# Optimization experiments

Hardware: AMD Instinct MI355X
Metric: run time of the kernel (lower is better)

## Reference

```python
import jax, jax.numpy as jnp
import numpy as np

T, B, I, H = 2048, 512, 10, 20  # seq_len, batch, input_size, hidden_size
G = 4 * H  # gate dim, PyTorch order: i, f, g, o


def _lstm_scan(x, w_ih, w_hh, b_ih, b_hh):
    # x: [T, B, I]; w_ih: [4H, I]; w_hh: [4H, H]; biases: [4H]
    # Precompute input projection for all timesteps (one big GEMM).
    x_proj = jnp.einsum('tbi,gi->tbg', x, w_ih) + b_ih + b_hh  # [T, B, 4H]

    def step(carry, xg):
        h, c = carry
        gates = xg + h @ w_hh.T  # [B, 4H]
        i, f, g, o = jnp.split(gates, 4, axis=-1)
        i = jax.nn.sigmoid(i)
        f = jax.nn.sigmoid(f)
        g = jnp.tanh(g)
        o = jax.nn.sigmoid(o)
        c = f * c + i * g
        h = o * jnp.tanh(c)
        return (h, c), h

    h0 = jnp.zeros((x.shape[1], H), x.dtype)
    c0 = jnp.zeros((x.shape[1], H), x.dtype)
    _, hs = jax.lax.scan(step, (h0, c0), x_proj)
    return hs  # [T, B, H]


def setup_inputs() -> dict:
    key = jax.random.key(0)
    ks = jax.random.split(key, 9)
    s_ih = 1.0 / np.sqrt(H)
    inp = {
        'x': jax.random.normal(ks[0], (T, B, I, 1), dtype=jnp.float32),
        'w_ih_f': jax.random.uniform(ks[1], (G, I), jnp.float32, -s_ih, s_ih),
        'w_hh_f': jax.random.uniform(ks[2], (G, H), jnp.float32, -s_ih, s_ih),
        'b_ih_f': jax.random.uniform(ks[3], (G,), jnp.float32, -s_ih, s_ih),
        'b_hh_f': jax.random.uniform(ks[4], (G,), jnp.float32, -s_ih, s_ih),
        'w_ih_r': jax.random.uniform(ks[5], (G, I), jnp.float32, -s_ih, s_ih),
        'w_hh_r': jax.random.uniform(ks[6], (G, H), jnp.float32, -s_ih, s_ih),
        'b_ih_r': jax.random.uniform(ks[7], (G,), jnp.float32, -s_ih, s_ih),
        'b_hh_r': jax.random.uniform(ks[8], (G,), jnp.float32, -s_ih, s_ih),
    }
    return inp


def reference(x, w_ih_f, w_hh_f, b_ih_f, b_hh_f, w_ih_r, w_hh_r, b_ih_r, b_hh_r):
    xs = jnp.squeeze(x, -1)  # [T, B, I]
    out_f = _lstm_scan(xs, w_ih_f, w_hh_f, b_ih_f, b_hh_f)            # forward dir
    out_r = _lstm_scan(xs[::-1], w_ih_r, w_hh_r, b_ih_r, b_hh_r)[::-1]  # reverse dir
    return jnp.concatenate([out_f, out_r], axis=-1)  # [T, B, 2H]
```

## Files before the change

kernel.cpp:

```cpp
#include <hip/hip_runtime.h>

typedef float f2 __attribute__((ext_vector_type(2)));
typedef float f4 __attribute__((ext_vector_type(4)));

#define TT 2048
#define BB 512
#define II 10
#define HH 20
#define CH 16
#define RS 32
#define NCHUNK (TT / CH)

#define LOG2E 1.44269504088896340736f

__device__ __forceinline__ float fexp2(float x) {
#if __has_builtin(__builtin_amdgcn_exp2f)
    return __builtin_amdgcn_exp2f(x);
#else
    return exp2f(x);
#endif
}

__global__ __launch_bounds__(128) void lstm_bidir(
    const float* __restrict__ x,
    const float* __restrict__ w_ih_f, const float* __restrict__ w_hh_f,
    const float* __restrict__ b_ih_f, const float* __restrict__ b_hh_f,
    const float* __restrict__ w_ih_r, const float* __restrict__ w_hh_r,
    const float* __restrict__ b_ih_r, const float* __restrict__ b_hh_r,
    float* __restrict__ out)
{
    const int tid  = threadIdx.x;
    const int wid  = tid >> 6;
    const int lane = tid & 63;
    const int s    = blockIdx.x;

    const int  dirh = lane >> 5;
    const int  hl   = lane & 31;
    const bool valid = (hl < HH);
    const int  j     = valid ? hl : (HH - 1);

    const float* __restrict__ w_ih = dirh ? w_ih_r : w_ih_f;
    const float* __restrict__ w_hh = dirh ? w_hh_r : w_hh_f;
    const float* __restrict__ b_ih = dirh ? b_ih_r : b_ih_f;
    const float* __restrict__ b_hh = dirh ? b_hh_r : b_hh_f;

    const int t0    = dirh ? (TT - 1) : 0;
    const int xstep = dirh ? -(BB * II) : (BB * II);
    const int ostep = dirh ? -(BB * 2 * HH) : (BB * 2 * HH);
    const int xbase = (t0 * BB + s) * II;

    const float gsc[4] = { -LOG2E, -LOG2E, -2.0f * LOG2E, -LOG2E };

    __shared__ f4    ring[RS][64];
    __shared__ float hstage[CH * 64];

    if (wid == 1) {
        f2 wih[4][5];
        float bs[4];
#pragma unroll
        for (int g = 0; g < 4; ++g) {
            const int r = g * HH + j;
#pragma unroll
            for (int k = 0; k < 5; ++k) {
                f2 w = *(const f2*)(w_ih + r * II + 2 * k);
                wih[g][k] = w * gsc[g];
            }
            bs[g] = (b_ih[r] + b_hh[r]) * gsc[g];
        }

        auto produce8 = [&](int base) {
            f2 xb[8][5];
#pragma unroll
            for (int i = 0; i < 8; ++i) {
                int u = base + i; if (u > TT - 1) u = TT - 1;
                const float* px = x + (xbase + u * xstep);
#pragma unroll
                for (int k = 0; k < 5; ++k) xb[i][k] = *(const f2*)(px + 2 * k);
            }
#pragma unroll
            for (int i = 0; i < 8; ++i) {
                const int u = base + i;
                if (u < TT) {
                    f4 xp;
#pragma unroll
                    for (int g = 0; g < 4; ++g) {
                        f2 p = {bs[g], 0.f};
#pragma unroll
                        for (int k = 0; k < 5; ++k) p += wih[g][k] * xb[i][k];
                        xp[g] = p[0] + p[1];
                    }
                    ring[u & (RS - 1)][lane] = xp;
                }
            }
        };

        produce8(0);
        produce8(8);
        for (int chunk = 0; chunk < NCHUNK; ++chunk) {
            __syncthreads();
            const int base = (chunk + 1) * CH;
            produce8(base);
            produce8(base + 8);
        }
    } else {
        __builtin_amdgcn_s_setprio(1);

        f2 whh[4][10];
#pragma unroll
        for (int g = 0; g < 4; ++g) {
            const int r = g * HH + j;
#pragma unroll
            for (int k = 0; k < 10; ++k) {
                f2 w = *(const f2*)(w_hh + r * HH + 2 * k);
                whh[g][k] = w * gsc[g];
            }
        }

        const int obase = (t0 * BB + s) * (2 * HH) + dirh * HH;
        int offd[10], lds_d[10];
#pragma unroll
        for (int q = 0; q < 10; ++q) {
            const int idx = q * 32 + hl;
            const int td  = idx / HH;
            const int jd  = idx - td * HH;
            offd[q]  = obase + td * ostep + jd;
            lds_d[q] = td * 64 + dirh * 32 + jd;
        }

        const int hboff = dirh * 32;

        f4 hb[5];
#pragma unroll
        for (int k = 0; k < 5; ++k) hb[k] = f4{0.f, 0.f, 0.f, 0.f};

        float c = 0.0f, h = 0.0f;
        int t = 0;

        for (int chunk = 0; chunk < NCHUNK; ++chunk) {
            __syncthreads();
            f4 xp = ring[t & (RS - 1)][lane];
#pragma unroll
            for (int i = 0; i < CH; ++i, ++t) {
                f2 a0[4], a1[4];
#pragma unroll
                for (int g = 0; g < 4; ++g) { a0[g] = f2{0.f, 0.f}; a1[g] = f2{0.f, 0.f}; }
#pragma unroll
                for (int k = 0; k < 5; ++k) {
                    const f4 hv = hb[k];
                    f2 lo; lo[0] = hv[0]; lo[1] = hv[1];
                    f2 hi; hi[0] = hv[2]; hi[1] = hv[3];
#pragma unroll
                    for (int g = 0; g < 4; ++g) {
                        a0[g] += whh[g][2 * k]     * lo;
                        a1[g] += whh[g][2 * k + 1] * hi;
                    }
                }
                float u[4];
#pragma unroll
                for (int g = 0; g < 4; ++g) {
                    const f2 a = a0[g] + a1[g];
                    u[g] = (xp[g] + a[0]) + a[1];
                }

                const float ig = __builtin_amdgcn_rcpf(1.0f + fexp2(u[0]));
                const float fg = __builtin_amdgcn_rcpf(1.0f + fexp2(u[1]));
                const float sg = __builtin_amdgcn_rcpf(1.0f + fexp2(u[2]));
                const float og = __builtin_amdgcn_rcpf(1.0f + fexp2(u[3]));
                const float i2 = ig + ig;
                const float o2 = og + og;

                const float m = __builtin_fmaf(i2, sg, -ig);
                c = __builtin_fmaf(fg, c, m);
                const float sc_ = __builtin_amdgcn_rcpf(
                                    1.0f + fexp2(c * (-2.0f * LOG2E)));
                h = __builtin_fmaf(o2, sc_, -og);

                hstage[i * 64 + lane] = h;
                __builtin_amdgcn_wave_barrier();

#pragma unroll
                for (int k = 0; k < 5; ++k)
                    hb[k] = *(const f4*)&hstage[i * 64 + hboff + 4 * k];

                if (i < CH - 1) xp = ring[(t + 1) & (RS - 1)][lane];
            }

#pragma unroll
            for (int q = 0; q < 10; ++q) {
                const float v = hstage[lds_d[q]];
                out[offd[q]] = v;
                offd[q] += CH * ostep;
            }
        }
    }
}

extern "C" void kernel_launch(void* const* d_in, const int* in_sizes, int n_in,
                              void* d_out, int out_size, void* d_ws, size_t ws_size,
                              hipStream_t stream) {
    const float* xp     = (const float*)d_in[0];
    const float* w_ih_f = (const float*)d_in[1];
    const float* w_hh_f = (const float*)d_in[2];
    const float* b_ih_f = (const float*)d_in[3];
    const float* b_hh_f = (const float*)d_in[4];
    const float* w_ih_r = (const float*)d_in[5];
    const float* w_hh_r = (const float*)d_in[6];
    const float* b_ih_r = (const float*)d_in[7];
    const float* b_hh_r = (const float*)d_in[8];
    float* outp = (float*)d_out;

    hipLaunchKernelGGL(lstm_bidir, dim3(512), dim3(128), 0, stream,
                       xp, w_ih_f, w_hh_f, b_ih_f, b_hh_f,
                       w_ih_r, w_hh_r, b_ih_r, b_hh_r, outp);
}
```

Baseline: 506.7 us.

## Interleave forward and reverse LSTM recurrences within each lane of the consumer wave

Each consumer lane used to handle a single direction, with lanes 0-31 forward and 32-63 reverse. Now every lane computes both directions, holding both hidden weight sets (whhA/whhB) and staging each direction's h in its own LDS half. The two independent dependency chains are interleaved so one can hide the other's latency. The cost is roughly double the per-lane arithmetic, since all 64 lanes now do redundant work, plus heavier register pressure, and launch_bounds(128,1) is added to permit that.

```diff
diff --git a/kernel.cpp b/kernel.cpp
--- a/kernel.cpp
+++ b/kernel.cpp
@@ -21,7 +21,7 @@
 #endif
 }
 
-__global__ __launch_bounds__(128) void lstm_bidir(
+__global__ __launch_bounds__(128, 1) void lstm_bidir(
     const float* __restrict__ x,
     const float* __restrict__ w_ih_f, const float* __restrict__ w_hh_f,
     const float* __restrict__ b_ih_f, const float* __restrict__ b_hh_f,
@@ -34,27 +34,23 @@
     const int lane = tid & 63;
     const int s    = blockIdx.x;
 
-    const int  dirh = lane >> 5;
-    const int  hl   = lane & 31;
-    const bool valid = (hl < HH);
-    const int  j     = valid ? hl : (HH - 1);
-
-    const float* __restrict__ w_ih = dirh ? w_ih_r : w_ih_f;
-    const float* __restrict__ w_hh = dirh ? w_hh_r : w_hh_f;
-    const float* __restrict__ b_ih = dirh ? b_ih_r : b_ih_f;
-    const float* __restrict__ b_hh = dirh ? b_hh_r : b_hh_f;
-
-    const int t0    = dirh ? (TT - 1) : 0;
-    const int xstep = dirh ? -(BB * II) : (BB * II);
-    const int ostep = dirh ? -(BB * 2 * HH) : (BB * 2 * HH);
-    const int xbase = (t0 * BB + s) * II;
+    const bool valid = ((lane & 31) < HH);
+    const int  j     = valid ? (lane & 31) : (HH - 1);
 
     const float gsc[4] = { -LOG2E, -LOG2E, -2.0f * LOG2E, -LOG2E };
 
     __shared__ f4    ring[RS][64];
-    __shared__ float hstage[CH * 64];
+    __shared__ float hstage[2 * CH * 64];
 
     if (wid == 1) {
+        const int dirh = lane >> 5;
+        const float* __restrict__ w_ih = dirh ? w_ih_r : w_ih_f;
+        const float* __restrict__ b_ih = dirh ? b_ih_r : b_ih_f;
+        const float* __restrict__ b_hh = dirh ? b_hh_r : b_hh_f;
+        const int t0    = dirh ? (TT - 1) : 0;
+        const int xstep = dirh ? -(BB * II) : (BB * II);
+        const int xbase = (t0 * BB + s) * II;
+
         f2 wih[4][5];
         float bs[4];
 #pragma unroll
@@ -105,91 +101,109 @@
     } else {
         __builtin_amdgcn_s_setprio(1);
 
-        f2 whh[4][10];
+        f2 whhA[4][10], whhB[4][10];
 #pragma unroll
         for (int g = 0; g < 4; ++g) {
             const int r = g * HH + j;
 #pragma unroll
             for (int k = 0; k < 10; ++k) {
-                f2 w = *(const f2*)(w_hh + r * HH + 2 * k);
-                whh[g][k] = w * gsc[g];
-            }
-        }
-
-        const int obase = (t0 * BB + s) * (2 * HH) + dirh * HH;
-        int offd[10], lds_d[10];
-#pragma unroll
-        for (int q = 0; q < 10; ++q) {
-            const int idx = q * 32 + hl;
-            const int td  = idx / HH;
-            const int jd  = idx - td * HH;
-            offd[q]  = obase + td * ostep + jd;
-            lds_d[q] = td * 64 + dirh * 32 + jd;
-        }
-
-        const int hboff = dirh * 32;
-
-        f4 hb[5];
-#pragma unroll
-        for (int k = 0; k < 5; ++k) hb[k] = f4{0.f, 0.f, 0.f, 0.f};
-
-        float c = 0.0f, h = 0.0f;
+                f2 wA = *(const f2*)(w_hh_f + r * HH + 2 * k);
+                f2 wB = *(const f2*)(w_hh_r + r * HH + 2 * k);
+                whhA[g][k] = wA * gsc[g];
+                whhB[g][k] = wB * gsc[g];
+            }
+        }
+
+        const int ostepF = BB * 2 * HH;
+        const int ostepR = -ostepF;
+        const int obaseF = s * 2 * HH;
+        const int obaseR = ((TT - 1) * BB + s) * 2 * HH + HH;
+
+        auto comp = [&](const f2 (&whh)[4][10], const f4 (&hb)[5], const f4& xp,
+                        float& c, float& h) {
+            f2 a0[4], a1[4];
+#pragma unroll
+            for (int g = 0; g < 4; ++g) { a0[g] = f2{xp[g], 0.f}; a1[g] = f2{0.f, 0.f}; }
+#pragma unroll
+            for (int k = 0; k < 5; ++k) {
+                const f4 hv = hb[k];
+                f2 lo; lo[0] = hv[0]; lo[1] = hv[1];
+                f2 hi; hi[0] = hv[2]; hi[1] = hv[3];
+#pragma unroll
+                for (int g = 0; g < 4; ++g) {
+                    a0[g] += whh[g][2 * k]     * lo;
+                    a1[g] += whh[g][2 * k + 1] * hi;
+                }
+            }
+            float u[4];
+#pragma unroll
+            for (int g = 0; g < 4; ++g) {
+                const f2 a = a0[g] + a1[g];
+                u[g] = a[0] + a[1];
+            }
+            const float ig = __builtin_amdgcn_rcpf(1.0f + fexp2(u[0]));
+            const float fg = __builtin_amdgcn_rcpf(1.0f + fexp2(u[1]));
+            const float sg = __builtin_amdgcn_rcpf(1.0f + fexp2(u[2]));
+            const float og = __builtin_amdgcn_rcpf(1.0f + fexp2(u[3]));
+            const float i2 = ig + ig;
+            const float o2 = og + og;
+            const float m  = __builtin_fmaf(i2, sg, -ig);
+            c = __builtin_fmaf(fg, c, m);
+            const float sc_ = __builtin_amdgcn_rcpf(
+                                1.0f + fexp2(c * (-2.0f * LOG2E)));
+            h = __builtin_fmaf(o2, sc_, -og);
+        };
+
+        hstage[CH * 64 + (CH - 1) * 64 + lane] = 0.0f;
+
+        f4 hbA[5], hbB[5];
+#pragma unroll
+        for (int k = 0; k < 5; ++k) hbA[k] = f4{0.f, 0.f, 0.f, 0.f};
+
+        float cA = 0.f, hA = 0.f, cB = 0.f, hB = 0.f;
         int t = 0;
 
         for (int chunk = 0; chunk < NCHUNK; ++chunk) {
             __syncthreads();
-            f4 xp = ring[t & (RS - 1)][lane];
+            f4 xpA = ring[t & (RS - 1)][j];
+            f4 xpB = ring[t & (RS - 1)][32 + j];
 #pragma unroll
             for (int i = 0; i < CH; ++i, ++t) {
-                f2 a0[4], a1[4];
-#pragma unroll
-                for (int g = 0; g < 4; ++g) { a0[g] = f2{0.f, 0.f}; a1[g] = f2{0.f, 0.f}; }
-#pragma unroll
-                for (int k = 0; k < 5; ++k) {
-                    const f4 hv = hb[k];
-                    f2 lo; lo[0] = hv[0]; lo[1] = hv[1];
-                    f2 hi; hi[0] = hv[2]; hi[1] = hv[3];
-#pragma unroll
-                    for (int g = 0; g < 4; ++g) {
-                        a0[g] += whh[g][2 * k]     * lo;
-                        a1[g] += whh[g][2 * k + 1] * hi;
-                    }
+#pragma unroll
+                for (int k = 0; k < 5; ++k)
+                    hbB[k] = *(const f4*)&hstage[CH * 64 + (((i + CH - 1) & (CH - 1)) * 64) + 4 * k];
+
+                comp(whhA, hbA, xpA, cA, hA);
+
+                hstage[i * 64 + lane] = hA;
+                __builtin_amdgcn_wave_barrier();
+
+#pragma unroll
+                for (int k = 0; k < 5; ++k)
+                    hbA[k] = *(const f4*)&hstage[i * 64 + 4 * k];
+
+                comp(whhB, hbB, xpB, cB, hB);
+
+                hstage[CH * 64 + i * 64 + lane] = hB;
+                __builtin_amdgcn_wave_barrier();
+
+                if (i < CH - 1) {
+                    xpA = ring[(t + 1) & (RS - 1)][j];
+                    xpB = ring[(t + 1) & (RS - 1)][32 + j];
                 }
-                float u[4];
-#pragma unroll
-                for (int g = 0; g < 4; ++g) {
-                    const f2 a = a0[g] + a1[g];
-                    u[g] = (xp[g] + a[0]) + a[1];
-                }
-
-                const float ig = __builtin_amdgcn_rcpf(1.0f + fexp2(u[0]));
-                const float fg = __builtin_amdgcn_rcpf(1.0f + fexp2(u[1]));
-                const float sg = __builtin_amdgcn_rcpf(1.0f + fexp2(u[2]));
-                const float og = __builtin_amdgcn_rcpf(1.0f + fexp2(u[3]));
-                const float i2 = ig + ig;
-                const float o2 = og + og;
-
-                const float m = __builtin_fmaf(i2, sg, -ig);
-                c = __builtin_fmaf(fg, c, m);
-                const float sc_ = __builtin_amdgcn_rcpf(
-                                    1.0f + fexp2(c * (-2.0f * LOG2E)));
-                h = __builtin_fmaf(o2, sc_, -og);
-
-                hstage[i * 64 + lane] = h;
-                __builtin_amdgcn_wave_barrier();
-
-#pragma unroll
-                for (int k = 0; k < 5; ++k)
-                    hb[k] = *(const f4*)&hstage[i * 64 + hboff + 4 * k];
-
-                if (i < CH - 1) xp = ring[(t + 1) & (RS - 1)][lane];
             }
 
 #pragma unroll
             for (int q = 0; q < 10; ++q) {
-                const float v = hstage[lds_d[q]];
-                out[offd[q]] = v;
-                offd[q] += CH * ostep;
+                const int sc  = q / 5;
+                const int idx = (q % 5) * 64 + lane;
+                const int td  = idx / HH;
+                const int jd  = idx - td * HH;
+                const float v = hstage[sc * CH * 64 + td * 64 + jd];
+                const int tglob = chunk * CH + td;
+                const int o = sc ? (obaseR + tglob * ostepR + jd)
+                                 : (obaseF + tglob * ostepF + jd);
+                out[o] = v;
             }
         }
     }
```

Result: slower. 780.3 us (+54.0%).

## Process two batch sequences per block with interleaved recurrences for ILP

Applied to the files above, without the earlier changes.

Each block now handles two batch elements, so grid size halves to 256 blocks. The compute wave runs two independent LSTM recurrences in alternation, letting one chain's dependent latency (LDS round-trip, transcendentals) overlap with the other's arithmetic. The input projection is also folded into the accumulator init, and the output store is reorganised to write both sequences' rows together. The cost is twice the serial work per wave, so the kernel only gains if the interleaving hides enough of each step's latency, and the halved grid may leave CUs idle.

```diff
diff --git a/kernel.cpp b/kernel.cpp
--- a/kernel.cpp
+++ b/kernel.cpp
@@ -21,7 +21,7 @@
 #endif
 }
 
-__global__ __launch_bounds__(128) void lstm_bidir(
+__global__ __launch_bounds__(128, 1) void lstm_bidir(
     const float* __restrict__ x,
     const float* __restrict__ w_ih_f, const float* __restrict__ w_hh_f,
     const float* __restrict__ b_ih_f, const float* __restrict__ b_hh_f,
@@ -32,12 +32,19 @@
     const int tid  = threadIdx.x;
     const int wid  = tid >> 6;
     const int lane = tid & 63;
-    const int s    = blockIdx.x;
-
-    const int  dirh = lane >> 5;
-    const int  hl   = lane & 31;
+    const int blk  = blockIdx.x;
+    const int sA   = 2 * blk;
+    const int sB   = 2 * blk + 1;
+
+    const int  dirh  = lane >> 5;
+    const int  hl    = lane & 31;
     const bool valid = (hl < HH);
     const int  j     = valid ? hl : (HH - 1);
+
+    const float gsc[4] = { -LOG2E, -LOG2E, -2.0f * LOG2E, -LOG2E };
+
+    __shared__ f4    ring[RS][2][64];
+    __shared__ float hstage[2][CH][64];
 
     const float* __restrict__ w_ih = dirh ? w_ih_r : w_ih_f;
     const float* __restrict__ w_hh = dirh ? w_hh_r : w_hh_f;
@@ -46,13 +53,6 @@
 
     const int t0    = dirh ? (TT - 1) : 0;
     const int xstep = dirh ? -(BB * II) : (BB * II);
-    const int ostep = dirh ? -(BB * 2 * HH) : (BB * 2 * HH);
-    const int xbase = (t0 * BB + s) * II;
-
-    const float gsc[4] = { -LOG2E, -LOG2E, -2.0f * LOG2E, -LOG2E };
-
-    __shared__ f4    ring[RS][64];
-    __shared__ float hstage[CH * 64];
 
     if (wid == 1) {
         f2 wih[4][5];
@@ -67,8 +67,10 @@
             }
             bs[g] = (b_ih[r] + b_hh[r]) * gsc[g];
         }
-
-        auto produce8 = [&](int base) {
+        const int xbaseA = (t0 * BB + sA) * II;
+        const int xbaseB = xbaseA + II;
+
+        auto produce8 = [&](int sc, int xbase, int base) {
             f2 xb[8][5];
 #pragma unroll
             for (int i = 0; i < 8; ++i) {
@@ -89,18 +91,18 @@
                         for (int k = 0; k < 5; ++k) p += wih[g][k] * xb[i][k];
                         xp[g] = p[0] + p[1];
                     }
-                    ring[u & (RS - 1)][lane] = xp;
+                    ring[u & (RS - 1)][sc][lane] = xp;
                 }
             }
         };
 
-        produce8(0);
-        produce8(8);
+        produce8(0, xbaseA, 0); produce8(0, xbaseA, 8);
+        produce8(1, xbaseB, 0); produce8(1, xbaseB, 8);
         for (int chunk = 0; chunk < NCHUNK; ++chunk) {
             __syncthreads();
             const int base = (chunk + 1) * CH;
-            produce8(base);
-            produce8(base + 8);
+            produce8(0, xbaseA, base); produce8(0, xbaseA, base + 8);
+            produce8(1, xbaseB, base); produce8(1, xbaseB, base + 8);
         }
     } else {
         __builtin_amdgcn_s_setprio(1);
@@ -116,80 +118,87 @@
             }
         }
 
-        const int obase = (t0 * BB + s) * (2 * HH) + dirh * HH;
-        int offd[10], lds_d[10];
-#pragma unroll
-        for (int q = 0; q < 10; ++q) {
-            const int idx = q * 32 + hl;
-            const int td  = idx / HH;
-            const int jd  = idx - td * HH;
-            offd[q]  = obase + td * ostep + jd;
-            lds_d[q] = td * 64 + dirh * 32 + jd;
-        }
-
         const int hboff = dirh * 32;
 
-        f4 hb[5];
-#pragma unroll
-        for (int k = 0; k < 5; ++k) hb[k] = f4{0.f, 0.f, 0.f, 0.f};
-
-        float c = 0.0f, h = 0.0f;
+        auto comp = [&](const f4 (&hb)[5], const f4& xp, float& c, float& h) {
+            f2 a0[4], a1[4];
+#pragma unroll
+            for (int g = 0; g < 4; ++g) { a0[g] = f2{xp[g], 0.f}; a1[g] = f2{0.f, 0.f}; }
+#pragma unroll
+            for (int k = 0; k < 5; ++k) {
+                const f4 hv = hb[k];
+                f2 lo; lo[0] = hv[0]; lo[1] = hv[1];
+                f2 hi; hi[0] = hv[2]; hi[1] = hv[3];
+#pragma unroll
+                for (int g = 0; g < 4; ++g) {
+                    a0[g] += whh[g][2 * k]     * lo;
+                    a1[g] += whh[g][2 * k + 1] * hi;
+                }
+            }
+            float u[4];
+#pragma unroll
+            for (int g = 0; g < 4; ++g) {
+                const f2 a = a0[g] + a1[g];
+                u[g] = a[0] + a[1];
+            }
+            const float ig = __builtin_amdgcn_rcpf(1.0f + fexp2(u[0]));
+            const float fg = __builtin_amdgcn_rcpf(1.0f + fexp2(u[1]));
+            const float sg = __builtin_amdgcn_rcpf(1.0f + fexp2(u[2]));
+            const float og = __builtin_amdgcn_rcpf(1.0f + fexp2(u[3]));
+            const float i2 = ig + ig;
+            const float o2 = og + og;
+            const float m  = __builtin_fmaf(i2, sg, -ig);
+            c = __builtin_fmaf(fg, c, m);
+            const float sc_ = __builtin_amdgcn_rcpf(
+                                1.0f + fexp2(c * (-2.0f * LOG2E)));
+            h = __builtin_fmaf(o2, sc_, -og);
+        };
+
+        f4 hbA[5], hbB[5];
+#pragma unroll
+        for (int k = 0; k < 5; ++k) { hbA[k] = f4{0.f,0.f,0.f,0.f}; hbB[k] = f4{0.f,0.f,0.f,0.f}; }
+
+        float cA = 0.f, hA = 0.f, cB = 0.f, hB = 0.f;
         int t = 0;
 
         for (int chunk = 0; chunk < NCHUNK; ++chunk) {
             __syncthreads();
-            f4 xp = ring[t & (RS - 1)][lane];
-#pragma unroll
+            f4 xpA = ring[t & (RS - 1)][0][lane];
+            f4 xpB = ring[t & (RS - 1)][1][lane];
+#pragma unroll 4
             for (int i = 0; i < CH; ++i, ++t) {
-                f2 a0[4], a1[4];
-#pragma unroll
-                for (int g = 0; g < 4; ++g) { a0[g] = f2{0.f, 0.f}; a1[g] = f2{0.f, 0.f}; }
-#pragma unroll
-                for (int k = 0; k < 5; ++k) {
-                    const f4 hv = hb[k];
-                    f2 lo; lo[0] = hv[0]; lo[1] = hv[1];
-                    f2 hi; hi[0] = hv[2]; hi[1] = hv[3];
-#pragma unroll
-                    for (int g = 0; g < 4; ++g) {
-                        a0[g] += whh[g][2 * k]     * lo;
-                        a1[g] += whh[g][2 * k + 1] * hi;
-                    }
-                }
-                float u[4];
-#pragma unroll
-                for (int g = 0; g < 4; ++g) {
-                    const f2 a = a0[g] + a1[g];
-                    u[g] = (xp[g] + a[0]) + a[1];
-                }
-
-                const float ig = __builtin_amdgcn_rcpf(1.0f + fexp2(u[0]));
-                const float fg = __builtin_amdgcn_rcpf(1.0f + fexp2(u[1]));
-                const float sg = __builtin_amdgcn_rcpf(1.0f + fexp2(u[2]));
-                const float og = __builtin_amdgcn_rcpf(1.0f + fexp2(u[3]));
-                const float i2 = ig + ig;
-                const float o2 = og + og;
-
-                const float m = __builtin_fmaf(i2, sg, -ig);
-                c = __builtin_fmaf(fg, c, m);
-                const float sc_ = __builtin_amdgcn_rcpf(
-                                    1.0f + fexp2(c * (-2.0f * LOG2E)));
-                h = __builtin_fmaf(o2, sc_, -og);
-
-                hstage[i * 64 + lane] = h;
+                comp(hbA, xpA, cA, hA);
+                hstage[0][i][lane] = hA;
                 __builtin_amdgcn_wave_barrier();
-
 #pragma unroll
                 for (int k = 0; k < 5; ++k)
-                    hb[k] = *(const f4*)&hstage[i * 64 + hboff + 4 * k];
-
-                if (i < CH - 1) xp = ring[(t + 1) & (RS - 1)][lane];
-            }
-
+                    hbA[k] = *(const f4*)&hstage[0][i][hboff + 4 * k];
+                if (i < CH - 1) xpA = ring[(t + 1) & (RS - 1)][0][lane];
+
+                comp(hbB, xpB, cB, hB);
+                hstage[1][i][lane] = hB;
+                __builtin_amdgcn_wave_barrier();
+#pragma unroll
+                for (int k = 0; k < 5; ++k)
+                    hbB[k] = *(const f4*)&hstage[1][i][hboff + 4 * k];
+                if (i < CH - 1) xpB = ring[(t + 1) & (RS - 1)][1][lane];
+            }
+
+            const int tbase = chunk * CH;
 #pragma unroll
             for (int q = 0; q < 10; ++q) {
-                const float v = hstage[lds_d[q]];
-                out[offd[q]] = v;
-                offd[q] += CH * ostep;
+                const int idx = q * 64 + lane;
+                const int td  = idx / 40;
+                const int r   = idx - td * 40;
+                const int dd  = r / 20;
+                const int jd  = r - dd * 20;
+                const int tg  = tbase + td;
+                const int trow = dd ? (TT - 1 - tg) : tg;
+                const int oA = (trow * BB + sA) * (2 * HH) + dd * HH + jd;
+                const float vA = hstage[0][td][dd * 32 + jd];
+                const float vB = hstage[1][td][dd * 32 + jd];
+                out[oA]            = vA;
+                out[oA + 2 * HH]   = vB;
             }
         }
     }
@@ -209,7 +218,7 @@
     const float* b_hh_r = (const float*)d_in[8];
     float* outp = (float*)d_out;
 
-    hipLaunchKernelGGL(lstm_bidir, dim3(512), dim3(128), 0, stream,
+    hipLaunchKernelGGL(lstm_bidir, dim3(256), dim3(128), 0, stream,
                        xp, w_ih_f, w_hh_f, b_ih_f, b_hh_f,
                        w_ih_r, w_hh_r, b_ih_r, b_hh_r, outp);
 }
```

Result: slower. 921.7 us (+81.9%).
